# Kernel tuning notes

Measured on AMD Instinct MI355X. Metric: run time of the kernel, lower is better.

Reference implementation:

```python
import jax, jax.numpy as jnp
import numpy as np

N_LOWF, N_HIGHF, E, D, L = 100000, 100000, 1600000, 32, 2
EPS = 1e-5
SLOPE = 0.2  # GATv2 default negative_slope


def _segment_softmax(e, seg, n):
    m = jax.ops.segment_max(e, seg, num_segments=n)
    m = jnp.where(jnp.isfinite(m), m, 0.0)
    ex = jnp.exp(e - m[seg])
    s = jax.ops.segment_sum(ex, seg, num_segments=n)
    return ex / (s[seg] + 1e-16)


def _gcn(x, src, dst, n, W, b):
    # GCNConv with add_self_loops=True, normalize=True (PyG defaults)
    h = x @ W  # [n, D]
    deg = jax.ops.segment_sum(jnp.ones(src.shape[0], x.dtype), dst, num_segments=n) + 1.0
    dinv = jax.lax.rsqrt(deg)
    msg = h[src] * (dinv[src] * dinv[dst])[:, None]  # [E, D]
    out = jax.ops.segment_sum(msg, dst, num_segments=n)
    out = out + h * (1.0 / deg)[:, None]  # self-loop term deg^-1
    return out + b


def _gatv2(x_src, x_dst, src, dst, n_dst, Wl, Wr, att, b):
    # GATv2Conv, heads=1, add_self_loops=False
    hl = x_src @ Wl  # [n_src, D]
    hr = x_dst @ Wr  # [n_dst, D]
    e = jax.nn.leaky_relu(hl[src] + hr[dst], SLOPE) @ att  # [E]
    alpha = _segment_softmax(e, dst, n_dst)
    out = jax.ops.segment_sum(hl[src] * alpha[:, None], dst, num_segments=n_dst)
    return out + b


def _bn(x, g, b):
    mu = jnp.mean(x, axis=0)
    var = jnp.mean(jnp.square(x - mu), axis=0)
    return g * (x - mu) * jax.lax.rsqrt(var + EPS) + b


def _forward(x_lowf, x_highf, gcn_ll_W, gcn_ll_b, gcn_hh_W, gcn_hh_b,
             gat_hl_Wl, gat_hl_Wr, gat_hl_att, gat_hl_b,
             gat_lh_Wl, gat_lh_Wr, gat_lh_att, gat_lh_b,
             bn_lowf_gamma, bn_lowf_beta, bn_highf_gamma, bn_highf_beta,
             ei_ll, ei_hh, ei_hl, ei_lh):
    xl, xh = x_lowf, x_highf
    for i in range(L):
        # HeteroConv with aggr='sum' over relations targeting each node type
        new_l = (_gcn(xl, ei_ll[0], ei_ll[1], N_LOWF, gcn_ll_W[i], gcn_ll_b[i])
                 + _gatv2(xh, xl, ei_hl[0], ei_hl[1], N_LOWF,
                          gat_hl_Wl[i], gat_hl_Wr[i], gat_hl_att[i], gat_hl_b[i]))
        new_h = (_gcn(xh, ei_hh[0], ei_hh[1], N_HIGHF, gcn_hh_W[i], gcn_hh_b[i])
                 + _gatv2(xl, xh, ei_lh[0], ei_lh[1], N_HIGHF,
                          gat_lh_Wl[i], gat_lh_Wr[i], gat_lh_att[i], gat_lh_b[i]))
        # per-node-type BatchNorm + ReLU (dropout = identity in eval)
        xl = jax.nn.relu(_bn(new_l, bn_lowf_gamma[i], bn_lowf_beta[i]))
        xh = jax.nn.relu(_bn(new_h, bn_highf_gamma[i], bn_highf_beta[i]))
    return jnp.concatenate([xl, xh], axis=0)  # [N_LOWF+N_HIGHF, D]


def setup_inputs() -> dict:
    key = jax.random.key(0)
    ks = jax.random.split(key, 32)
    rn = lambda i, s: jax.random.normal(ks[i], s, dtype=jnp.float32) * 0.1
    ri = lambda i, n: jax.random.randint(ks[i], (2, E), 0, n, dtype=jnp.int64)
    return {
        "x_lowf": rn(0, (N_LOWF, D)),
        "x_highf": rn(1, (N_HIGHF, D)),
        "gcn_ll_W": rn(2, (L, D, D)), "gcn_ll_b": jnp.zeros((L, D), jnp.float32),
        "gcn_hh_W": rn(3, (L, D, D)), "gcn_hh_b": jnp.zeros((L, D), jnp.float32),
        "gat_hl_Wl": rn(4, (L, D, D)), "gat_hl_Wr": rn(5, (L, D, D)),
        "gat_hl_att": rn(6, (L, D)), "gat_hl_b": jnp.zeros((L, D), jnp.float32),
        "gat_lh_Wl": rn(7, (L, D, D)), "gat_lh_Wr": rn(8, (L, D, D)),
        "gat_lh_att": rn(9, (L, D)), "gat_lh_b": jnp.zeros((L, D), jnp.float32),
        "bn_lowf_gamma": jnp.ones((L, D), jnp.float32), "bn_lowf_beta": jnp.zeros((L, D), jnp.float32),
        "bn_highf_gamma": jnp.ones((L, D), jnp.float32), "bn_highf_beta": jnp.zeros((L, D), jnp.float32),
        "ei_ll": ri(10, N_LOWF),
        "ei_hh": ri(11, N_HIGHF),
        "ei_hl": jnp.stack([jax.random.randint(ks[12], (E,), 0, N_HIGHF, dtype=jnp.int64),
                            jax.random.randint(ks[13], (E,), 0, N_LOWF, dtype=jnp.int64)]),
        "ei_lh": jnp.stack([jax.random.randint(ks[14], (E,), 0, N_LOWF, dtype=jnp.int64),
                            jax.random.randint(ks[15], (E,), 0, N_HIGHF, dtype=jnp.int64)]),
    }


def reference(x_lowf, x_highf, gcn_ll_W, gcn_ll_b, gcn_hh_W, gcn_hh_b,
              gat_hl_Wl, gat_hl_Wr, gat_hl_att, gat_hl_b,
              gat_lh_Wl, gat_lh_Wr, gat_lh_att, gat_lh_b,
              bn_lowf_gamma, bn_lowf_beta, bn_highf_gamma, bn_highf_beta,
              ei_ll, ei_hh, ei_hl, ei_lh):
    return _forward(x_lowf, x_highf, gcn_ll_W, gcn_ll_b, gcn_hh_W, gcn_hh_b,
                    gat_hl_Wl, gat_hl_Wr, gat_hl_att, gat_hl_b,
                    gat_lh_Wl, gat_lh_Wr, gat_lh_att, gat_lh_b,
                    bn_lowf_gamma, bn_lowf_beta, bn_highf_gamma, bn_highf_beta,
                    ei_ll, ei_hh, ei_hl, ei_lh)
```

## Files before the change

### kernel.cpp

```cpp
#include <hip/hip_runtime.h>
#include <hip/hip_fp16.h>

#define NN 100000
#define EDG 1600000
#define LAY 2
#define NBKT 98
#define BKTPAD 128
#define CAP 18432
#define PCHUNK 2560
#define CPR 625

static inline int cdiv(int a, int b) { return (a + b - 1) / b; }

__global__ void k_init(int* bhist, float* stats) {
    int t = blockIdx.x * blockDim.x + threadIdx.x;
    if (t < 4 * BKTPAD) bhist[t] = 0;
    if (t < 4 * 64) stats[t] = 0.f;
}

__global__ __launch_bounds__(256) void k_bhist(const int* __restrict__ ll,
                                               const int* __restrict__ hh,
                                               const int* __restrict__ hl,
                                               const int* __restrict__ lh, int* __restrict__ bhist) {
    __shared__ int h[NBKT];
    int tid = threadIdx.x;
    if (tid < NBKT) h[tid] = 0;
    __syncthreads();
    int r = blockIdx.x / CPR;
    int chunk = blockIdx.x - r * CPR;
    const int* dst = (r == 0 ? ll : r == 1 ? hh : r == 2 ? hl : lh) + EDG;
    int base = chunk * PCHUNK;
#pragma unroll
    for (int k = 0; k < 10; k++) {
        int d = dst[base + k * 256 + tid];
        atomicAdd(&h[d >> 10], 1);
    }
    __syncthreads();
    if (tid < NBKT) atomicAdd(&bhist[r * BKTPAD + tid], h[tid]);
}

__global__ void k_bscan(const int* __restrict__ bhist, int* __restrict__ bases,
                        int* __restrict__ gcursor, int* __restrict__ rp) {
    __shared__ int sh[BKTPAD];
    int t = threadIdx.x;
    for (int r = 0; r < 4; r++) {
        int v = (t < BKTPAD) ? ((t < NBKT) ? bhist[r * BKTPAD + t] : 0) : 0;
        if (t < BKTPAD) sh[t] = v;
        __syncthreads();
        for (int off = 1; off < BKTPAD; off <<= 1) {
            int x = (t < BKTPAD && t >= off) ? sh[t - off] : 0;
            __syncthreads();
            if (t < BKTPAD) sh[t] += x;
            __syncthreads();
        }
        if (t < BKTPAD) {
            int ex = sh[t] - v;
            bases[r * BKTPAD + t] = ex;
            gcursor[r * BKTPAD + t] = ex;
        }
        __syncthreads();
    }
    if (t < 4) rp[t * (NN + 1) + NN] = EDG;
}

__global__ __launch_bounds__(256) void k_partition(const int* __restrict__ ll,
                                                   const int* __restrict__ hh,
                                                   const int* __restrict__ hl,
                                                   const int* __restrict__ lh,
                                                   int* __restrict__ gcursor,
                                                   unsigned* __restrict__ pairs) {
    __shared__ int lhist[NBKT], lbase[NBKT];
    int tid = threadIdx.x;
    if (tid < NBKT) lhist[tid] = 0;
    __syncthreads();
    int r = blockIdx.x / CPR;
    int chunk = blockIdx.x - r * CPR;
    const int* ei = (r == 0 ? ll : r == 1 ? hh : r == 2 ? hl : lh);
    const int* srcp = ei;
    const int* dstp = ei + EDG;
    int base = chunk * PCHUNK;
    int s[10], d[10], rk[10];
#pragma unroll
    for (int k = 0; k < 10; k++) {
        int e = base + k * 256 + tid;
        s[k] = srcp[e];
        d[k] = dstp[e];
        rk[k] = atomicAdd(&lhist[d[k] >> 10], 1);
    }
    __syncthreads();
    if (tid < NBKT) lbase[tid] = atomicAdd(&gcursor[r * BKTPAD + tid], lhist[tid]);
    __syncthreads();
    unsigned* pr = pairs + (size_t)r * EDG;
#pragma unroll
    for (int k = 0; k < 10; k++) {
        int b = d[k] >> 10;
        unsigned w = ((unsigned)(d[k] & 1023) << 22) | (unsigned)s[k];
        pr[lbase[b] + rk[k]] = w;
    }
}

__global__ __launch_bounds__(256) void k_build(const unsigned* __restrict__ pairs,
                                               const int* __restrict__ bases,
                                               const int* __restrict__ bhist, int* __restrict__ rp,
                                               int* __restrict__ cs, float* __restrict__ dinv_l,
                                               float* __restrict__ dinv_h) {
    __shared__ int cnt_arr[1024];
    __shared__ int sh[256];
    __shared__ int srcs[CAP];
    int tid = threadIdx.x;
    int r = blockIdx.x / NBKT;
    int b = blockIdx.x - r * NBKT;
    int base = bases[r * BKTPAD + b];
    int cnt = bhist[r * BKTPAD + b];
    int d0 = b << 10;
    int ndst = NN - d0;
    if (ndst > 1024) ndst = 1024;
#pragma unroll
    for (int j = 0; j < 4; j++) cnt_arr[4 * tid + j] = 0;
    __syncthreads();
    const unsigned* pr = pairs + (size_t)r * EDG + base;
    for (int i = tid; i < cnt; i += 256) {
        unsigned w = pr[i];
        atomicAdd(&cnt_arr[w >> 22], 1);
    }
    __syncthreads();
    int c0 = cnt_arr[4 * tid], c1 = cnt_arr[4 * tid + 1], c2 = cnt_arr[4 * tid + 2],
        c3 = cnt_arr[4 * tid + 3];
    int s = c0 + c1 + c2 + c3;
    sh[tid] = s;
    __syncthreads();
    for (int off = 1; off < 256; off <<= 1) {
        int x = (tid >= off) ? sh[tid - off] : 0;
        __syncthreads();
        sh[tid] += x;
        __syncthreads();
    }
    int run = sh[tid] - s;
    int st0 = run, st1 = st0 + c0, st2 = st1 + c1, st3 = st2 + c2;
    cnt_arr[4 * tid] = st0;
    cnt_arr[4 * tid + 1] = st1;
    cnt_arr[4 * tid + 2] = st2;
    cnt_arr[4 * tid + 3] = st3;
    int* rpr = rp + r * (NN + 1);
    if (4 * tid + 0 < ndst) rpr[d0 + 4 * tid + 0] = base + st0;
    if (4 * tid + 1 < ndst) rpr[d0 + 4 * tid + 1] = base + st1;
    if (4 * tid + 2 < ndst) rpr[d0 + 4 * tid + 2] = base + st2;
    if (4 * tid + 3 < ndst) rpr[d0 + 4 * tid + 3] = base + st3;
    if (r < 2) {
        float* dv = (r == 0) ? dinv_l : dinv_h;
        if (4 * tid + 0 < ndst) dv[d0 + 4 * tid + 0] = rsqrtf((float)c0 + 1.f);
        if (4 * tid + 1 < ndst) dv[d0 + 4 * tid + 1] = rsqrtf((float)c1 + 1.f);
        if (4 * tid + 2 < ndst) dv[d0 + 4 * tid + 2] = rsqrtf((float)c2 + 1.f);
        if (4 * tid + 3 < ndst) dv[d0 + 4 * tid + 3] = rsqrtf((float)c3 + 1.f);
    }
    __syncthreads();
    for (int i = tid; i < cnt; i += 256) {
        unsigned w = pr[i];
        int pos = atomicAdd(&cnt_arr[w >> 22], 1);
        if (pos < CAP) srcs[pos] = (int)(w & 0x3FFFFFu);
    }
    __syncthreads();
    int* csr = cs + (size_t)r * EDG + base;
    for (int i = tid; i < cnt; i += 256) csr[i] = (i < CAP) ? srcs[i] : 0;
}

__global__ __launch_bounds__(256) void k_gemm3(const float* __restrict__ x,
                                               const float* __restrict__ stats,
                                               const float* __restrict__ gamma,
                                               const float* __restrict__ beta,
                                               const float* __restrict__ W0,
                                               const float* __restrict__ W1,
                                               const float* __restrict__ W2,
                                               const float* __restrict__ scale0,
                                               __half* __restrict__ y0, __half* __restrict__ y1,
                                               __half* __restrict__ y2) {
    __shared__ float Ws[3][1024];
    __shared__ float xs[8][32];
    int tid = threadIdx.x;
    for (int i = tid; i < 1024; i += 256) {
        Ws[0][i] = W0[i];
        Ws[1][i] = W1[i];
        Ws[2][i] = W2[i];
    }
    int c = tid & 31, rl = tid >> 5;
    float mu = 0.f, gs = 1.f, be = 0.f;
    if (stats) {
        const float inv_n = 1.f / (float)NN;
        mu = stats[c] * inv_n;
        float var = stats[32 + c] * inv_n - mu * mu;
        gs = gamma[c] * rsqrtf(var + 1e-5f);
        be = beta[c];
    }
    for (int r0 = blockIdx.x * 8; r0 < NN; r0 += gridDim.x * 8) {
        int r = r0 + rl;
        __syncthreads();
        if (r < NN) {
            float xv = x[(size_t)r * 32 + c];
            if (stats) {
                xv = gs * (xv - mu) + be;
                xv = (xv > 0.f) ? xv : 0.f;
            }
            xs[rl][c] = xv;
        }
        __syncthreads();
        if (r < NN) {
            float a0 = 0.f, a1 = 0.f, a2 = 0.f;
#pragma unroll
            for (int k = 0; k < 32; k++) {
                float xv = xs[rl][k];
                a0 += xv * Ws[0][k * 32 + c];
                a1 += xv * Ws[1][k * 32 + c];
                a2 += xv * Ws[2][k * 32 + c];
            }
            a0 *= scale0[r];
            y0[(size_t)r * 32 + c] = __float2half(a0);
            y1[(size_t)r * 32 + c] = __float2half(a1);
            y2[(size_t)r * 32 + c] = __float2half(a2);
        }
    }
}

__device__ inline void cvt8(int4 r, float2* f) {
    const __half2* h = (const __half2*)&r;
    f[0] = __half22float2(h[0]);
    f[1] = __half22float2(h[1]);
    f[2] = __half22float2(h[2]);
    f[3] = __half22float2(h[3]);
}

__global__ __launch_bounds__(256) void k_aggregate(
    const int* __restrict__ rp_gcn, const int* __restrict__ cs_gcn,
    const __half* __restrict__ h_gcn, const float* __restrict__ dinv,
    const int* __restrict__ rp_gat, const int* __restrict__ cs_gat,
    const __half* __restrict__ h_gl, const __half* __restrict__ h_gr,
    const float* __restrict__ attv, const float* __restrict__ b_gcn,
    const float* __restrict__ b_gat, float* __restrict__ out, float* __restrict__ stats) {
    int tid = threadIdx.x;
    int c4 = tid & 3;
    int g = tid >> 2;
    int v = blockIdx.x * 64 + g;
    bool alive = v < NN;

    const int4* hg4 = (const int4*)h_gcn;
    const int4* hl4 = (const int4*)h_gl;
    const int4* hr4p = (const int4*)h_gr;
    const float2* at2 = (const float2*)attv;

    float2 a[4];
#pragma unroll
    for (int q = 0; q < 4; q++) a[q] = at2[c4 * 4 + q];

    float2 res[4];
#pragma unroll
    for (int q = 0; q < 4; q++) res[q] = make_float2(0.f, 0.f);

    if (alive) {
        const int4 zero4 = make_int4(0, 0, 0, 0);
        float2 acc[4];
#pragma unroll
        for (int q = 0; q < 4; q++) acc[q] = make_float2(0.f, 0.f);
        int b0 = rp_gcn[v], e0 = rp_gcn[v + 1];
        for (int e = b0; e < e0; e += 4) {
            int myi = cs_gcn[min(e + c4, e0 - 1)];
            int4 raw[4];
#pragma unroll
            for (int j = 0; j < 4; j++) {
                int sj = __shfl(myi, j, 4);
                raw[j] = ((e + j) < e0) ? hg4[(size_t)sj * 4 + c4] : zero4;
            }
#pragma unroll
            for (int j = 0; j < 4; j++) {
                float2 f[4];
                cvt8(raw[j], f);
#pragma unroll
                for (int q = 0; q < 4; q++) {
                    acc[q].x += f[q].x;
                    acc[q].y += f[q].y;
                }
            }
        }
        {
            int4 selfr = hg4[(size_t)v * 4 + c4];
            float2 f[4];
            cvt8(selfr, f);
#pragma unroll
            for (int q = 0; q < 4; q++) {
                acc[q].x += f[q].x;
                acc[q].y += f[q].y;
            }
        }
        float dv = dinv[v];
        float2 hr[4];
        {
            int4 rr = hr4p[(size_t)v * 4 + c4];
            cvt8(rr, hr);
        }
        float m = -3.0e38f, ss = 0.f;
        float2 o[4];
#pragma unroll
        for (int q = 0; q < 4; q++) o[q] = make_float2(0.f, 0.f);
        int b1 = rp_gat[v], e1 = rp_gat[v + 1];
        for (int e = b1; e < e1; e += 4) {
            int myi = cs_gat[min(e + c4, e1 - 1)];
            int4 raw[4];
#pragma unroll
            for (int j = 0; j < 4; j++) {
                int sj = __shfl(myi, j, 4);
                raw[j] = hl4[(size_t)sj * 4 + c4];
            }
            float p[4];
#pragma unroll
            for (int j = 0; j < 4; j++) {
                float2 f[4];
                cvt8(raw[j], f);
                float pj = 0.f;
#pragma unroll
                for (int q = 0; q < 4; q++) {
                    float tx = f[q].x + hr[q].x;
                    tx = (tx > 0.f) ? tx : 0.2f * tx;
                    float ty = f[q].y + hr[q].y;
                    ty = (ty > 0.f) ? ty : 0.2f * ty;
                    pj += tx * a[q].x + ty * a[q].y;
                }
                p[j] = pj;
            }
#pragma unroll
            for (int off = 1; off <= 2; off <<= 1) {
#pragma unroll
                for (int j = 0; j < 4; j++) p[j] += __shfl_xor(p[j], off, 4);
            }
#pragma unroll
            for (int j = 0; j < 4; j++)
                if ((e + j) >= e1) p[j] = -3.0e38f;
            float cmax = fmaxf(fmaxf(p[0], p[1]), fmaxf(p[2], p[3]));
            float mn = fmaxf(m, cmax);
            float sc = __expf(m - mn);
            float wsum = 0.f;
            float2 oa[4];
#pragma unroll
            for (int q = 0; q < 4; q++) oa[q] = make_float2(0.f, 0.f);
#pragma unroll
            for (int j = 0; j < 4; j++) {
                float w = __expf(p[j] - mn);
                wsum += w;
                float2 f[4];
                cvt8(raw[j], f);
#pragma unroll
                for (int q = 0; q < 4; q++) {
                    oa[q].x += w * f[q].x;
                    oa[q].y += w * f[q].y;
                }
            }
            ss = ss * sc + wsum;
#pragma unroll
            for (int q = 0; q < 4; q++) {
                o[q].x = o[q].x * sc + oa[q].x;
                o[q].y = o[q].y * sc + oa[q].y;
            }
            m = mn;
        }
        float inv = 1.f / (ss + 1e-16f);
#pragma unroll
        for (int q = 0; q < 4; q++) {
            float bx = b_gcn[c4 * 8 + 2 * q] + b_gat[c4 * 8 + 2 * q];
            float by = b_gcn[c4 * 8 + 2 * q + 1] + b_gat[c4 * 8 + 2 * q + 1];
            res[q].x = acc[q].x * dv + o[q].x * inv + bx;
            res[q].y = acc[q].y * dv + o[q].y * inv + by;
        }
        float4* o4 = (float4*)(out + (size_t)v * 32 + c4 * 8);
        o4[0] = make_float4(res[0].x, res[0].y, res[1].x, res[1].y);
        o4[1] = make_float4(res[2].x, res[2].y, res[3].x, res[3].y);
    }
    float s1[8], s2[8];
#pragma unroll
    for (int q = 0; q < 4; q++) {
        s1[2 * q] = res[q].x;
        s1[2 * q + 1] = res[q].y;
        s2[2 * q] = res[q].x * res[q].x;
        s2[2 * q + 1] = res[q].y * res[q].y;
    }
#pragma unroll
    for (int off = 4; off <= 32; off <<= 1) {
#pragma unroll
        for (int k = 0; k < 8; k++) {
            s1[k] += __shfl_xor(s1[k], off, 64);
            s2[k] += __shfl_xor(s2[k], off, 64);
        }
    }
    __shared__ float sst[4][2][32];
    int wave = tid >> 6, lane = tid & 63;
    if (lane < 4) {
#pragma unroll
        for (int k = 0; k < 8; k++) {
            sst[wave][0][lane * 8 + k] = s1[k];
            sst[wave][1][lane * 8 + k] = s2[k];
        }
    }
    __syncthreads();
    if (tid < 64) {
        int which = tid >> 5, col = tid & 31;
        float t = sst[0][which][col] + sst[1][which][col] + sst[2][which][col] +
                  sst[3][which][col];
        atomicAdd(&stats[which * 32 + col], t);
    }
}

__global__ void k_bn_apply(const float* __restrict__ x, const float* __restrict__ stats,
                           const float* __restrict__ gamma, const float* __restrict__ beta,
                           float* __restrict__ y) {
    int total4 = NN * 8;
    const float inv_n = 1.f / (float)NN;
    const float4* x4 = (const float4*)x;
    float4* y4 = (float4*)y;
    for (int i = blockIdx.x * blockDim.x + threadIdx.x; i < total4; i += gridDim.x * blockDim.x) {
        int c0 = (i * 4) & 31;
        float4 v = x4[i];
        float r[4] = {v.x, v.y, v.z, v.w};
#pragma unroll
        for (int j = 0; j < 4; j++) {
            int c = c0 + j;
            float mu = stats[c] * inv_n;
            float var = stats[32 + c] * inv_n - mu * mu;
            float gs = gamma[c] * rsqrtf(var + 1e-5f);
            float t = gs * (r[j] - mu) + beta[c];
            r[j] = (t > 0.f) ? t : 0.f;
        }
        y4[i] = make_float4(r[0], r[1], r[2], r[3]);
    }
}

extern "C" void kernel_launch(void* const* d_in, const int* in_sizes, int n_in, void* d_out,
                              int out_size, void* d_ws, size_t ws_size, hipStream_t stream) {
    const float* x_l = (const float*)d_in[0];
    const float* x_h = (const float*)d_in[1];
    const float* Wll = (const float*)d_in[2];
    const float* bll = (const float*)d_in[3];
    const float* Whh = (const float*)d_in[4];
    const float* bhh = (const float*)d_in[5];
    const float* Whl_l = (const float*)d_in[6];
    const float* Whl_r = (const float*)d_in[7];
    const float* att_hl = (const float*)d_in[8];
    const float* b_hl = (const float*)d_in[9];
    const float* Wlh_l = (const float*)d_in[10];
    const float* Wlh_r = (const float*)d_in[11];
    const float* att_lh = (const float*)d_in[12];
    const float* b_lh = (const float*)d_in[13];
    const float* g_l = (const float*)d_in[14];
    const float* be_l = (const float*)d_in[15];
    const float* g_h = (const float*)d_in[16];
    const float* be_h = (const float*)d_in[17];
    const int* ei_ll = (const int*)d_in[18];
    const int* ei_hh = (const int*)d_in[19];
    const int* ei_hl = (const int*)d_in[20];
    const int* ei_lh = (const int*)d_in[21];

    char* p = (char*)d_ws;
    auto alloc = [&](size_t bytes) -> void* {
        void* r = (void*)p;
        p += (bytes + 255) & ~(size_t)255;
        return r;
    };
    const size_t HFEAT = (size_t)NN * 32 * sizeof(__half);
    const size_t FFEAT = (size_t)NN * 32 * sizeof(float);
    unsigned* pairs = (unsigned*)alloc((size_t)4 * EDG * sizeof(unsigned));
    float* new_l = (float*)pairs;
    float* new_h = (float*)((char*)pairs + FFEAT);
    __half* hgcn_l = (__half*)alloc(HFEAT);
    __half* hgcn_h = (__half*)alloc(HFEAT);
    __half* hgl_hl = (__half*)alloc(HFEAT);
    __half* hgr_hl = (__half*)alloc(HFEAT);
    __half* hgl_lh = (__half*)alloc(HFEAT);
    __half* hgr_lh = (__half*)alloc(HFEAT);
    int* cs = (int*)alloc((size_t)4 * EDG * sizeof(int));
    int* rp = (int*)alloc((size_t)4 * (NN + 1) * sizeof(int));
    float* dinv_l = (float*)alloc(NN * sizeof(float));
    float* dinv_h = (float*)alloc(NN * sizeof(float));
    int* bhist = (int*)alloc(4 * BKTPAD * sizeof(int));
    int* bases = (int*)alloc(4 * BKTPAD * sizeof(int));
    int* gcursor = (int*)alloc(4 * BKTPAD * sizeof(int));
    float* stats = (float*)alloc(4 * 64 * sizeof(float));

    const int TB = 256;
    k_init<<<2, TB, 0, stream>>>(bhist, stats);
    k_bhist<<<4 * CPR, TB, 0, stream>>>(ei_ll, ei_hh, ei_hl, ei_lh, bhist);
    k_bscan<<<1, TB, 0, stream>>>(bhist, bases, gcursor, rp);
    k_partition<<<4 * CPR, TB, 0, stream>>>(ei_ll, ei_hh, ei_hl, ei_lh, gcursor, pairs);
    k_build<<<4 * NBKT, TB, 0, stream>>>(pairs, bases, bhist, rp, cs, dinv_l, dinv_h);

    const int* rp0 = rp;
    const int* rp1 = rp + (NN + 1);
    const int* rp2 = rp + 2 * (NN + 1);
    const int* rp3 = rp + 3 * (NN + 1);
    const int* cs0 = cs;
    const int* cs1 = cs + (size_t)EDG;
    const int* cs2 = cs + (size_t)2 * EDG;
    const int* cs3 = cs + (size_t)3 * EDG;

    const int GRID = 2048;
    const int AGRID = cdiv(NN, 64);
    float* st0l = stats;
    float* st0h = stats + 64;
    float* st1l = stats + 128;
    float* st1h = stats + 192;

    k_gemm3<<<GRID, TB, 0, stream>>>(x_l, nullptr, nullptr, nullptr, Wll, Whl_r, Wlh_l, dinv_l,
                                     hgcn_l, hgr_hl, hgl_lh);
    k_gemm3<<<GRID, TB, 0, stream>>>(x_h, nullptr, nullptr, nullptr, Whh, Wlh_r, Whl_l, dinv_h,
                                     hgcn_h, hgr_lh, hgl_hl);
    k_aggregate<<<AGRID, TB, 0, stream>>>(rp0, cs0, hgcn_l, dinv_l, rp2, cs2, hgl_hl, hgr_hl,
                                          att_hl, bll, b_hl, new_l, st0l);
    k_aggregate<<<AGRID, TB, 0, stream>>>(rp1, cs1, hgcn_h, dinv_h, rp3, cs3, hgl_lh, hgr_lh,
                                          att_lh, bhh, b_lh, new_h, st0h);
    k_gemm3<<<GRID, TB, 0, stream>>>(new_l, st0l, g_l, be_l, Wll + 1024, Whl_r + 1024,
                                     Wlh_l + 1024, dinv_l, hgcn_l, hgr_hl, hgl_lh);
    k_gemm3<<<GRID, TB, 0, stream>>>(new_h, st0h, g_h, be_h, Whh + 1024, Wlh_r + 1024,
                                     Whl_l + 1024, dinv_h, hgcn_h, hgr_lh, hgl_hl);
    k_aggregate<<<AGRID, TB, 0, stream>>>(rp0, cs0, hgcn_l, dinv_l, rp2, cs2, hgl_hl, hgr_hl,
                                          att_hl + 32, bll + 32, b_hl + 32, new_l, st1l);
    k_aggregate<<<AGRID, TB, 0, stream>>>(rp1, cs1, hgcn_h, dinv_h, rp3, cs3, hgl_lh, hgr_lh,
                                          att_lh + 32, bhh + 32, b_lh + 32, new_h, st1h);
    k_bn_apply<<<GRID, TB, 0, stream>>>(new_l, st1l, g_l + 32, be_l + 32, (float*)d_out);
    k_bn_apply<<<GRID, TB, 0, stream>>>(new_h, st1h, g_h + 32, be_h + 32,
                                        ((float*)d_out) + (size_t)NN * 32);
}
```

Before: 676.5 us.

## Drop histogram pass via fixed-capacity bucket slots; merge paired gemm and BN launches

Edge partitioning now writes into fixed-capacity per-bucket slots whose cursors start at preset offsets. That removes the separate destination-histogram kernel, which read every edge destination array once more, and its scan; a small scan after partitioning derives counts and bases from the final cursors. The two per-node-type projection GEMMs are merged into one launch by splitting blocks on the low bit of the block index. The two final BatchNorm-apply launches become a single kernel over the contiguous buffers. The risks are a larger pairs buffer and silent truncation if any bucket exceeds its slot capacity.

```diff
diff --git a/kernel.cpp b/kernel.cpp
--- a/kernel.cpp
+++ b/kernel.cpp
@@ -7,60 +7,19 @@
 #define NBKT 98
 #define BKTPAD 128
 #define CAP 18432
+#define CAPSLOT 18432
 #define PCHUNK 2560
 #define CPR 625
 
 static inline int cdiv(int a, int b) { return (a + b - 1) / b; }
 
-__global__ void k_init(int* bhist, float* stats) {
+__global__ void k_init2(int* gcursor, float* stats) {
     int t = blockIdx.x * blockDim.x + threadIdx.x;
-    if (t < 4 * BKTPAD) bhist[t] = 0;
+    if (t < 4 * BKTPAD) {
+        int r = t / BKTPAD, b = t - r * BKTPAD;
+        gcursor[t] = (b < NBKT) ? (r * NBKT + b) * CAPSLOT : 0;
+    }
     if (t < 4 * 64) stats[t] = 0.f;
-}
-
-__global__ __launch_bounds__(256) void k_bhist(const int* __restrict__ ll,
-                                               const int* __restrict__ hh,
-                                               const int* __restrict__ hl,
-                                               const int* __restrict__ lh, int* __restrict__ bhist) {
-    __shared__ int h[NBKT];
-    int tid = threadIdx.x;
-    if (tid < NBKT) h[tid] = 0;
-    __syncthreads();
-    int r = blockIdx.x / CPR;
-    int chunk = blockIdx.x - r * CPR;
-    const int* dst = (r == 0 ? ll : r == 1 ? hh : r == 2 ? hl : lh) + EDG;
-    int base = chunk * PCHUNK;
-#pragma unroll
-    for (int k = 0; k < 10; k++) {
-        int d = dst[base + k * 256 + tid];
-        atomicAdd(&h[d >> 10], 1);
-    }
-    __syncthreads();
-    if (tid < NBKT) atomicAdd(&bhist[r * BKTPAD + tid], h[tid]);
-}
-
-__global__ void k_bscan(const int* __restrict__ bhist, int* __restrict__ bases,
-                        int* __restrict__ gcursor, int* __restrict__ rp) {
-    __shared__ int sh[BKTPAD];
-    int t = threadIdx.x;
-    for (int r = 0; r < 4; r++) {
-        int v = (t < BKTPAD) ? ((t < NBKT) ? bhist[r * BKTPAD + t] : 0) : 0;
-        if (t < BKTPAD) sh[t] = v;
-        __syncthreads();
-        for (int off = 1; off < BKTPAD; off <<= 1) {
-            int x = (t < BKTPAD && t >= off) ? sh[t - off] : 0;
-            __syncthreads();
-            if (t < BKTPAD) sh[t] += x;
-            __syncthreads();
-        }
-        if (t < BKTPAD) {
-            int ex = sh[t] - v;
-            bases[r * BKTPAD + t] = ex;
-            gcursor[r * BKTPAD + t] = ex;
-        }
-        __syncthreads();
-    }
-    if (t < 4) rp[t * (NN + 1) + NN] = EDG;
 }
 
 __global__ __launch_bounds__(256) void k_partition(const int* __restrict__ ll,
@@ -90,18 +49,48 @@
     __syncthreads();
     if (tid < NBKT) lbase[tid] = atomicAdd(&gcursor[r * BKTPAD + tid], lhist[tid]);
     __syncthreads();
-    unsigned* pr = pairs + (size_t)r * EDG;
 #pragma unroll
     for (int k = 0; k < 10; k++) {
         int b = d[k] >> 10;
-        unsigned w = ((unsigned)(d[k] & 1023) << 22) | (unsigned)s[k];
-        pr[lbase[b] + rk[k]] = w;
-    }
+        int limit = (r * NBKT + b + 1) * CAPSLOT;
+        int pos = lbase[b] + rk[k];
+        if (pos < limit) {
+            unsigned w = ((unsigned)(d[k] & 1023) << 22) | (unsigned)s[k];
+            pairs[pos] = w;
+        }
+    }
+}
+
+__global__ void k_cscan(const int* __restrict__ gcursor, int* __restrict__ cnts,
+                        int* __restrict__ bases, int* __restrict__ rp) {
+    __shared__ int sh[BKTPAD];
+    int t = threadIdx.x;
+    for (int r = 0; r < 4; r++) {
+        int v = 0;
+        if (t < NBKT) {
+            v = gcursor[r * BKTPAD + t] - (r * NBKT + t) * CAPSLOT;
+            v = (v > CAPSLOT) ? CAPSLOT : v;
+        }
+        if (t < BKTPAD) sh[t] = v;
+        __syncthreads();
+        for (int off = 1; off < BKTPAD; off <<= 1) {
+            int x = (t < BKTPAD && t >= off) ? sh[t - off] : 0;
+            __syncthreads();
+            if (t < BKTPAD) sh[t] += x;
+            __syncthreads();
+        }
+        if (t < BKTPAD) {
+            cnts[r * BKTPAD + t] = v;
+            bases[r * BKTPAD + t] = sh[t] - v;
+        }
+        __syncthreads();
+    }
+    if (t < 4) rp[t * (NN + 1) + NN] = EDG;
 }
 
 __global__ __launch_bounds__(256) void k_build(const unsigned* __restrict__ pairs,
                                                const int* __restrict__ bases,
-                                               const int* __restrict__ bhist, int* __restrict__ rp,
+                                               const int* __restrict__ cnts, int* __restrict__ rp,
                                                int* __restrict__ cs, float* __restrict__ dinv_l,
                                                float* __restrict__ dinv_h) {
     __shared__ int cnt_arr[1024];
@@ -111,14 +100,14 @@
     int r = blockIdx.x / NBKT;
     int b = blockIdx.x - r * NBKT;
     int base = bases[r * BKTPAD + b];
-    int cnt = bhist[r * BKTPAD + b];
+    int cnt = cnts[r * BKTPAD + b];
     int d0 = b << 10;
     int ndst = NN - d0;
     if (ndst > 1024) ndst = 1024;
 #pragma unroll
     for (int j = 0; j < 4; j++) cnt_arr[4 * tid + j] = 0;
     __syncthreads();
-    const unsigned* pr = pairs + (size_t)r * EDG + base;
+    const unsigned* pr = pairs + (size_t)(r * NBKT + b) * CAPSLOT;
     for (int i = tid; i < cnt; i += 256) {
         unsigned w = pr[i];
         atomicAdd(&cnt_arr[w >> 22], 1);
@@ -164,18 +153,32 @@
     for (int i = tid; i < cnt; i += 256) csr[i] = (i < CAP) ? srcs[i] : 0;
 }
 
-__global__ __launch_bounds__(256) void k_gemm3(const float* __restrict__ x,
-                                               const float* __restrict__ stats,
-                                               const float* __restrict__ gamma,
-                                               const float* __restrict__ beta,
-                                               const float* __restrict__ W0,
-                                               const float* __restrict__ W1,
-                                               const float* __restrict__ W2,
-                                               const float* __restrict__ scale0,
-                                               __half* __restrict__ y0, __half* __restrict__ y1,
-                                               __half* __restrict__ y2) {
+__global__ __launch_bounds__(256) void k_gemm3x2(
+    const float* __restrict__ xa, const float* __restrict__ statsa,
+    const float* __restrict__ gammaa, const float* __restrict__ betaa,
+    const float* __restrict__ W0a, const float* __restrict__ W1a, const float* __restrict__ W2a,
+    const float* __restrict__ scalea, __half* __restrict__ y0a, __half* __restrict__ y1a,
+    __half* __restrict__ y2a, const float* __restrict__ xb, const float* __restrict__ statsb,
+    const float* __restrict__ gammab, const float* __restrict__ betab,
+    const float* __restrict__ W0b, const float* __restrict__ W1b, const float* __restrict__ W2b,
+    const float* __restrict__ scaleb, __half* __restrict__ y0b, __half* __restrict__ y1b,
+    __half* __restrict__ y2b) {
     __shared__ float Ws[3][1024];
     __shared__ float xs[8][32];
+    int sel = blockIdx.x & 1;
+    int bid = blockIdx.x >> 1;
+    int nb = gridDim.x >> 1;
+    const float* x = sel ? xb : xa;
+    const float* stats = sel ? statsb : statsa;
+    const float* gamma = sel ? gammab : gammaa;
+    const float* beta = sel ? betab : betaa;
+    const float* W0 = sel ? W0b : W0a;
+    const float* W1 = sel ? W1b : W1a;
+    const float* W2 = sel ? W2b : W2a;
+    const float* scale0 = sel ? scaleb : scalea;
+    __half* y0 = sel ? y0b : y0a;
+    __half* y1 = sel ? y1b : y1a;
+    __half* y2 = sel ? y2b : y2a;
     int tid = threadIdx.x;
     for (int i = tid; i < 1024; i += 256) {
         Ws[0][i] = W0[i];
@@ -191,7 +194,7 @@
         gs = gamma[c] * rsqrtf(var + 1e-5f);
         be = beta[c];
     }
-    for (int r0 = blockIdx.x * 8; r0 < NN; r0 += gridDim.x * 8) {
+    for (int r0 = bid * 8; r0 < NN; r0 += nb * 8) {
         int r = r0 + rl;
         __syncthreads();
         if (r < NN) {
@@ -405,14 +408,19 @@
     }
 }
 
-__global__ void k_bn_apply(const float* __restrict__ x, const float* __restrict__ stats,
-                           const float* __restrict__ gamma, const float* __restrict__ beta,
-                           float* __restrict__ y) {
-    int total4 = NN * 8;
+__global__ void k_bn2(const float* __restrict__ x, const float* __restrict__ stats_l,
+                      const float* __restrict__ stats_h, const float* __restrict__ gamma_l,
+                      const float* __restrict__ beta_l, const float* __restrict__ gamma_h,
+                      const float* __restrict__ beta_h, float* __restrict__ y) {
+    int total4 = 2 * NN * 8;
     const float inv_n = 1.f / (float)NN;
     const float4* x4 = (const float4*)x;
     float4* y4 = (float4*)y;
     for (int i = blockIdx.x * blockDim.x + threadIdx.x; i < total4; i += gridDim.x * blockDim.x) {
+        bool hi = i >= NN * 8;
+        const float* stats = hi ? stats_h : stats_l;
+        const float* gamma = hi ? gamma_h : gamma_l;
+        const float* beta = hi ? beta_h : beta_l;
         int c0 = (i * 4) & 31;
         float4 v = x4[i];
         float r[4] = {v.x, v.y, v.z, v.w};
@@ -462,7 +470,7 @@
     };
     const size_t HFEAT = (size_t)NN * 32 * sizeof(__half);
     const size_t FFEAT = (size_t)NN * 32 * sizeof(float);
-    unsigned* pairs = (unsigned*)alloc((size_t)4 * EDG * sizeof(unsigned));
+    unsigned* pairs = (unsigned*)alloc((size_t)4 * NBKT * CAPSLOT * sizeof(unsigned));
     float* new_l = (float*)pairs;
     float* new_h = (float*)((char*)pairs + FFEAT);
     __half* hgcn_l = (__half*)alloc(HFEAT);
@@ -475,17 +483,16 @@
     int* rp = (int*)alloc((size_t)4 * (NN + 1) * sizeof(int));
     float* dinv_l = (float*)alloc(NN * sizeof(float));
     float* dinv_h = (float*)alloc(NN * sizeof(float));
-    int* bhist = (int*)alloc(4 * BKTPAD * sizeof(int));
+    int* cnts = (int*)alloc(4 * BKTPAD * sizeof(int));
     int* bases = (int*)alloc(4 * BKTPAD * sizeof(int));
     int* gcursor = (int*)alloc(4 * BKTPAD * sizeof(int));
     float* stats = (float*)alloc(4 * 64 * sizeof(float));
 
     const int TB = 256;
-    k_init<<<2, TB, 0, stream>>>(bhist, stats);
-    k_bhist<<<4 * CPR, TB, 0, stream>>>(ei_ll, ei_hh, ei_hl, ei_lh, bhist);
-    k_bscan<<<1, TB, 0, stream>>>(bhist, bases, gcursor, rp);
+    k_init2<<<2, TB, 0, stream>>>(gcursor, stats);
     k_partition<<<4 * CPR, TB, 0, stream>>>(ei_ll, ei_hh, ei_hl, ei_lh, gcursor, pairs);
-    k_build<<<4 * NBKT, TB, 0, stream>>>(pairs, bases, bhist, rp, cs, dinv_l, dinv_h);
+    k_cscan<<<1, TB, 0, stream>>>(gcursor, cnts, bases, rp);
+    k_build<<<4 * NBKT, TB, 0, stream>>>(pairs, bases, cnts, rp, cs, dinv_l, dinv_h);
 
     const int* rp0 = rp;
     const int* rp1 = rp + (NN + 1);
@@ -503,23 +510,21 @@
     float* st1l = stats + 128;
     float* st1h = stats + 192;
 
-    k_gemm3<<<GRID, TB, 0, stream>>>(x_l, nullptr, nullptr, nullptr, Wll, Whl_r, Wlh_l, dinv_l,
-                                     hgcn_l, hgr_hl, hgl_lh);
-    k_gemm3<<<GRID, TB, 0, stream>>>(x_h, nullptr, nullptr, nullptr, Whh, Wlh_r, Whl_l, dinv_h,
-                                     hgcn_h, hgr_lh, hgl_hl);
+    k_gemm3x2<<<GRID, TB, 0, stream>>>(x_l, nullptr, nullptr, nullptr, Wll, Whl_r, Wlh_l, dinv_l,
+                                       hgcn_l, hgr_hl, hgl_lh, x_h, nullptr, nullptr, nullptr,
+                                       Whh, Wlh_r, Whl_l, dinv_h, hgcn_h, hgr_lh, hgl_hl);
     k_aggregate<<<AGRID, TB, 0, stream>>>(rp0, cs0, hgcn_l, dinv_l, rp2, cs2, hgl_hl, hgr_hl,
                                           att_hl, bll, b_hl, new_l, st0l);
     k_aggregate<<<AGRID, TB, 0, stream>>>(rp1, cs1, hgcn_h, dinv_h, rp3, cs3, hgl_lh, hgr_lh,
                                           att_lh, bhh, b_lh, new_h, st0h);
-    k_gemm3<<<GRID, TB, 0, stream>>>(new_l, st0l, g_l, be_l, Wll + 1024, Whl_r + 1024,
-                                     Wlh_l + 1024, dinv_l, hgcn_l, hgr_hl, hgl_lh);
-    k_gemm3<<<GRID, TB, 0, stream>>>(new_h, st0h, g_h, be_h, Whh + 1024, Wlh_r + 1024,
-                                     Whl_l + 1024, dinv_h, hgcn_h, hgr_lh, hgl_hl);
+    k_gemm3x2<<<GRID, TB, 0, stream>>>(new_l, st0l, g_l, be_l, Wll + 1024, Whl_r + 1024,
+                                       Wlh_l + 1024, dinv_l, hgcn_l, hgr_hl, hgl_lh, new_h, st0h,
+                                       g_h, be_h, Whh + 1024, Wlh_r + 1024, Whl_l + 1024, dinv_h,
+                                       hgcn_h, hgr_lh, hgl_hl);
     k_aggregate<<<AGRID, TB, 0, stream>>>(rp0, cs0, hgcn_l, dinv_l, rp2, cs2, hgl_hl, hgr_hl,
                                           att_hl + 32, bll + 32, b_hl + 32, new_l, st1l);
     k_aggregate<<<AGRID, TB, 0, stream>>>(rp1, cs1, hgcn_h, dinv_h, rp3, cs3, hgl_lh, hgr_lh,
                                           att_lh + 32, bhh + 32, b_lh + 32, new_h, st1h);
-    k_bn_apply<<<GRID, TB, 0, stream>>>(new_l, st1l, g_l + 32, be_l + 32, (float*)d_out);
-    k_bn_apply<<<GRID, TB, 0, stream>>>(new_h, st1h, g_h + 32, be_h + 32,
-                                        ((float*)d_out) + (size_t)NN * 32);
-}
+    k_bn2<<<GRID, TB, 0, stream>>>(new_l, st1l, st1h, g_l + 32, be_l + 32, g_h + 32, be_h + 32,
+                                   (float*)d_out);
+}
```

After: 639.9 us. -5.4%, faster.
